# Optimization experiments

Hardware: AMD Instinct MI355X
Metric: run time of the kernel (lower is better)

## Reference

```python
import jax, jax.numpy as jnp
import numpy as np

N = 262144          # num keyframes
E = 1048576         # num visual links (edges)
DT = 0.1            # IMU integration step
L1, L2, L3, L4 = 1.0, 0.5, 2.0, 0.5
EPS = 1e-6

# ---- quaternion helpers (pypose convention: q = [x, y, z, w]) ----

def qmul(q1, q2):
    v1, w1 = q1[..., :3], q1[..., 3:4]
    v2, w2 = q2[..., :3], q2[..., 3:4]
    w = w1 * w2 - jnp.sum(v1 * v2, axis=-1, keepdims=True)
    v = w1 * v2 + w2 * v1 + jnp.cross(v1, v2)
    return jnp.concatenate([v, w], axis=-1)

def qconj(q):
    return jnp.concatenate([-q[..., :3], q[..., 3:4]], axis=-1)

def qrot(q, x):
    # rotate vector x by unit quaternion q: x + 2*cross(v, cross(v,x) + w*x)
    v, w = q[..., :3], q[..., 3:4]
    return x + 2.0 * jnp.cross(v, jnp.cross(v, x) + w * x)

def so3_log(q):
    # log map of unit quaternion -> axis-angle phi (..., 3)
    v, w = q[..., :3], q[..., 3:4]
    n = jnp.linalg.norm(v, axis=-1, keepdims=True)
    n_safe = jnp.where(n < EPS, 1.0, n)
    theta = 2.0 * jnp.arctan2(n, w)
    w_safe = jnp.where(jnp.abs(w) < EPS, 1.0, w)
    factor = jnp.where(n < EPS, 2.0 / w_safe, theta / n_safe)
    return factor * v

def se3_inv(p):
    t, q = p[..., :3], p[..., 3:]
    qi = qconj(q)
    ti = -qrot(qi, t)
    return jnp.concatenate([ti, qi], axis=-1)

def se3_mul(p1, p2):
    t1, q1 = p1[..., :3], p1[..., 3:]
    t2, q2 = p2[..., :3], p2[..., 3:]
    t = t1 + qrot(q1, t2)
    return jnp.concatenate([t, qmul(q1, q2)], axis=-1)

def se3_log(p):
    # returns se(3) tensor [tau, phi] (pypose order) with tau = Jl^{-1}(phi) t
    t, q = p[..., :3], p[..., 3:]
    phi = so3_log(q)
    th = jnp.linalg.norm(phi, axis=-1, keepdims=True)
    th_safe = jnp.where(th < EPS, 1.0, th)
    coef = jnp.where(
        th < EPS,
        1.0 / 12.0 + th * th / 720.0,
        1.0 / (th_safe * th_safe)
        - (1.0 + jnp.cos(th_safe)) / (2.0 * th_safe * jnp.sin(th_safe)),
    )
    pxt = jnp.cross(phi, t)
    tau = t - 0.5 * pxt + coef * jnp.cross(phi, pxt)
    return jnp.concatenate([tau, phi], axis=-1)


def setup_inputs() -> dict:
    key = jax.random.key(0)
    ks = jax.random.split(key, 8)

    def unit_quat(k, n):
        q = jax.random.normal(k, (n, 4), dtype=jnp.float32)
        return q / jnp.linalg.norm(q, axis=-1, keepdims=True)

    pose = jnp.concatenate(
        [jax.random.normal(ks[0], (N, 3), dtype=jnp.float32),
         unit_quat(ks[1], N)], axis=-1)
    vel = jax.random.normal(ks[2], (N, 3), dtype=jnp.float32)
    vmot = jnp.concatenate(
        [0.1 * jax.random.normal(ks[3], (E, 3), dtype=jnp.float32),
         unit_quat(ks[4], E)], axis=-1)
    imu_drot = unit_quat(ks[5], N - 1)
    body_dvel = 0.1 * jax.random.normal(ks[6], (N - 1, 3), dtype=jnp.float32)
    body_dpos = 0.1 * jax.random.normal(ks[7], (N - 1, 3), dtype=jnp.float32)
    vlink = jax.random.randint(jax.random.fold_in(key, 99), (E, 2), 0, N)
    return dict(pose=pose, vel=vel, vmot=vmot, imu_drot=imu_drot,
                body_dvel=body_dvel, body_dpos=body_dpos, vlink=vlink)


def reference(pose, vel, vmot, imu_drot, body_dvel, body_dpos, vlink):
    trans, rot = pose[:, :3], pose[:, 3:]
    r1 = rot[:-1]

    # IMU model: world-frame increments (rotation-dependent, as in original)
    imu_dvel = qrot(r1, body_dvel)                      # world_dvel(pose.rotation())
    imu_dpos = qrot(r1, body_dpos) + vel[:-1] * DT      # world_dpos(rot, vel)

    # pose-graph residual: Log(vmot^{-1} @ pose1^{-1} @ pose2)  [E, 6]
    pose1 = pose[vlink[:, 0]]
    pose2 = pose[vlink[:, 1]]
    err = se3_mul(se3_inv(vmot), se3_mul(se3_inv(pose1), pose2))
    pgerr = se3_log(err)

    # adjacent velocity residual [N-1, 3]
    adjvelerr = imu_dvel - jnp.diff(vel, axis=0)

    # IMU rotation residual: Log(imu_drot @ R1^{-1} @ R2)  [N-1, 3]
    q_rel = qmul(imu_drot, qmul(qconj(rot[:-1]), rot[1:]))
    imuroterr = so3_log(q_rel)

    # translation/velocity residual [N-1, 3]
    transvelerr = imu_dpos - jnp.diff(trans, axis=0)

    return jnp.concatenate([
        L1 * pgerr.reshape(-1),
        L2 * adjvelerr.reshape(-1),
        L3 * imuroterr.reshape(-1),
        L4 * transvelerr.reshape(-1),
    ], axis=0)
```

## Files before the change

### kernel.cpp

```cpp
#include <hip/hip_runtime.h>
#include <math.h>

constexpr int   NN  = 262144;
constexpr int   NE  = 1048576;
constexpr float DTc = 0.1f;
constexpr float W1 = 1.0f, W2 = 0.5f, W3 = 2.0f, W4 = 0.5f;
constexpr float EPSc = 1e-6f;

typedef float    __attribute__((ext_vector_type(2))) f32x2;
typedef float    __attribute__((ext_vector_type(4))) f32x4;
typedef float    __attribute__((ext_vector_type(4), aligned(4))) f32x4u;
typedef float    __attribute__((ext_vector_type(2), aligned(4))) f32x2u;
typedef int      __attribute__((ext_vector_type(2))) i32x2;
typedef _Float16 __attribute__((ext_vector_type(8))) f16x8;

struct V3 { float x, y, z; };
struct Q4 { float x, y, z, w; };

__device__ __forceinline__ V3 v3(float x, float y, float z) { V3 r{x, y, z}; return r; }
__device__ __forceinline__ V3 vadd(V3 a, V3 b) { return v3(a.x + b.x, a.y + b.y, a.z + b.z); }
__device__ __forceinline__ V3 vsub(V3 a, V3 b) { return v3(a.x - b.x, a.y - b.y, a.z - b.z); }
__device__ __forceinline__ V3 vscale(float s, V3 a) { return v3(s * a.x, s * a.y, s * a.z); }
__device__ __forceinline__ V3 vcross(V3 a, V3 b) {
    return v3(a.y * b.z - a.z * b.y, a.z * b.x - a.x * b.z, a.x * b.y - a.y * b.x);
}
__device__ __forceinline__ float vdot(V3 a, V3 b) { return a.x * b.x + a.y * b.y + a.z * b.z; }

__device__ __forceinline__ Q4 qmul(Q4 a, Q4 b) {
    Q4 r;
    r.w = a.w * b.w - (a.x * b.x + a.y * b.y + a.z * b.z);
    r.x = a.w * b.x + b.w * a.x + (a.y * b.z - a.z * b.y);
    r.y = a.w * b.y + b.w * a.y + (a.z * b.x - a.x * b.z);
    r.z = a.w * b.z + b.w * a.z + (a.x * b.y - a.y * b.x);
    return r;
}
__device__ __forceinline__ Q4 qconj(Q4 q) { Q4 r{-q.x, -q.y, -q.z, q.w}; return r; }
__device__ __forceinline__ V3 qrot(Q4 q, V3 x) {
    V3 v = v3(q.x, q.y, q.z);
    V3 c1 = vadd(vcross(v, x), vscale(q.w, x));
    return vadd(x, vscale(2.0f, vcross(v, c1)));
}
__device__ __forceinline__ V3 so3_log(Q4 q) {
    V3 v = v3(q.x, q.y, q.z);
    float n = sqrtf(vdot(v, v));
    float theta = 2.0f * atan2f(n, q.w);
    float factor;
    if (n < EPSc) {
        float w_safe = (fabsf(q.w) < EPSc) ? 1.0f : q.w;
        factor = 2.0f / w_safe;
    } else {
        factor = theta / n;
    }
    return vscale(factor, v);
}

__device__ __forceinline__ void edge_residual(V3 tm, Q4 qm, V3 t1, Q4 q1,
                                              V3 t2, Q4 q2, float* __restrict__ o) {
    Q4 qa = qconj(q1);
    V3 ta = vscale(-1.0f, qrot(qa, t1));
    V3 tb = vadd(ta, qrot(qa, t2));
    Q4 qb = qmul(qa, q2);
    Q4 qc = qconj(qm);
    V3 tc = vscale(-1.0f, qrot(qc, tm));
    V3 te = vadd(tc, qrot(qc, tb));
    Q4 qe = qmul(qc, qb);

    V3 phi = so3_log(qe);
    float th = sqrtf(vdot(phi, phi));
    float coef;
    if (th < EPSc) {
        coef = 1.0f / 12.0f + th * th / 720.0f;
    } else {
        float s, c;
        sincosf(th, &s, &c);
        coef = 1.0f / (th * th) - (1.0f + c) / (2.0f * th * s);
    }
    V3 pxt = vcross(phi, te);
    V3 tau = vadd(vsub(te, vscale(0.5f, pxt)), vscale(coef, vcross(phi, pxt)));

    f32x2* o2 = (f32x2*)o;
    f32x2 a = {W1 * tau.x, W1 * tau.y};
    f32x2 b = {W1 * tau.z, W1 * phi.x};
    f32x2 c = {W1 * phi.y, W1 * phi.z};
    __builtin_nontemporal_store(a, o2);
    __builtin_nontemporal_store(b, o2 + 1);
    __builtin_nontemporal_store(c, o2 + 2);
}

__global__ __launch_bounds__(256) void node_pack_kernel(
    const float* __restrict__ pose, const float* __restrict__ vel,
    const float* __restrict__ imu_drot, const float* __restrict__ body_dvel,
    const float* __restrict__ body_dpos, f16x8* __restrict__ ppH,
    float* __restrict__ out)
{
    int i = blockIdx.x * blockDim.x + threadIdx.x;
    if (i >= NN) return;
    f32x4u pa0 = *(const f32x4u*)(pose + 7 * (size_t)i);
    f32x4u pa1 = *(const f32x4u*)(pose + 7 * (size_t)i + 3);
    f16x8 rec = {(_Float16)pa0.x, (_Float16)pa0.y, (_Float16)pa0.z,
                 (_Float16)pa1.x, (_Float16)pa1.y, (_Float16)pa1.z,
                 (_Float16)pa1.w, (_Float16)0.0f};
    ppH[i] = rec;
    if (i >= NN - 1) return;

    V3 tr1 = v3(pa0.x, pa0.y, pa0.z); Q4 r1 = {pa1.x, pa1.y, pa1.z, pa1.w};
    f32x4u pb0 = *(const f32x4u*)(pose + 7 * (size_t)(i + 1));
    f32x4u pb1 = *(const f32x4u*)(pose + 7 * (size_t)(i + 1) + 3);
    V3 tr2 = v3(pb0.x, pb0.y, pb0.z); Q4 r2 = {pb1.x, pb1.y, pb1.z, pb1.w};

    f32x4u vv = *(const f32x4u*)(vel + 3 * (size_t)i);
    f32x2u vw = *(const f32x2u*)(vel + 3 * (size_t)i + 4);
    V3 v1 = v3(vv.x, vv.y, vv.z);
    V3 v2 = v3(vv.w, vw.x, vw.y);
    V3 bdv = v3(body_dvel[3 * (size_t)i], body_dvel[3 * (size_t)i + 1], body_dvel[3 * (size_t)i + 2]);
    V3 bdp = v3(body_dpos[3 * (size_t)i], body_dpos[3 * (size_t)i + 1], body_dpos[3 * (size_t)i + 2]);
    f32x4 id4 = *(const f32x4*)(imu_drot + 4 * (size_t)i);
    Q4 idr = {id4.x, id4.y, id4.z, id4.w};

    V3 imu_dvel = qrot(r1, bdv);
    V3 adjvel = vsub(imu_dvel, vsub(v2, v1));
    Q4 qrel = qmul(idr, qmul(qconj(r1), r2));
    V3 imurot = so3_log(qrel);
    V3 imu_dpos = vadd(qrot(r1, bdp), vscale(DTc, v1));
    V3 transvel = vsub(imu_dpos, vsub(tr2, tr1));

    size_t base = (size_t)6 * NE;
    size_t nm1 = (size_t)(NN - 1);
    float* oa = out + base + 3 * (size_t)i;
    oa[0] = W2 * adjvel.x; oa[1] = W2 * adjvel.y; oa[2] = W2 * adjvel.z;
    float* ob = out + base + 3 * nm1 + 3 * (size_t)i;
    ob[0] = W3 * imurot.x; ob[1] = W3 * imurot.y; ob[2] = W3 * imurot.z;
    float* oc = out + base + 6 * nm1 + 3 * (size_t)i;
    oc[0] = W4 * transvel.x; oc[1] = W4 * transvel.y; oc[2] = W4 * transvel.z;
}

__global__ __launch_bounds__(256) void edge_kernel(
    const float* __restrict__ vmot, const int* __restrict__ vlink,
    const f16x8* __restrict__ ppH, float* __restrict__ out)
{
    __shared__ float smv[256 * 7];
    int e0 = blockIdx.x * 256;
    const f32x4* src = (const f32x4*)(vmot + (size_t)e0 * 7);
    {
        int idx = threadIdx.x;
        ((f32x4*)smv)[idx] = __builtin_nontemporal_load(src + idx);
        idx += 256;
        if (idx < 448) ((f32x4*)smv)[idx] = __builtin_nontemporal_load(src + idx);
    }
    int e = e0 + threadIdx.x;
    i32x2 l = __builtin_nontemporal_load((const i32x2*)vlink + e);
    f16x8 g1 = ppH[l.x];
    f16x8 g2 = ppH[l.y];
    __syncthreads();
    float m[7];
#pragma unroll
    for (int k = 0; k < 7; ++k) m[k] = smv[7 * threadIdx.x + k];

    V3 t1 = v3((float)g1[0], (float)g1[1], (float)g1[2]);
    Q4 q1 = {(float)g1[3], (float)g1[4], (float)g1[5], (float)g1[6]};
    V3 t2 = v3((float)g2[0], (float)g2[1], (float)g2[2]);
    Q4 q2 = {(float)g2[3], (float)g2[4], (float)g2[5], (float)g2[6]};

    edge_residual(v3(m[0], m[1], m[2]), Q4{m[3], m[4], m[5], m[6]},
                  t1, q1, t2, q2, out + 6 * (size_t)e);
}

__global__ __launch_bounds__(256) void vigraph_fallback(
    const float* __restrict__ pose, const float* __restrict__ vel,
    const float* __restrict__ vmot, const float* __restrict__ imu_drot,
    const float* __restrict__ body_dvel, const float* __restrict__ body_dpos,
    const int* __restrict__ vlink, float* __restrict__ out)
{
    int tid = blockIdx.x * blockDim.x + threadIdx.x;
    if (tid < NE) {
        int e = tid;
        const float* pm = vmot + 7 * (size_t)e;
        int i1 = vlink[2 * (size_t)e];
        int i2 = vlink[2 * (size_t)e + 1];
        const float* p1 = pose + 7 * (size_t)i1;
        const float* p2 = pose + 7 * (size_t)i2;
        edge_residual(v3(pm[0], pm[1], pm[2]), Q4{pm[3], pm[4], pm[5], pm[6]},
                      v3(p1[0], p1[1], p1[2]), Q4{p1[3], p1[4], p1[5], p1[6]},
                      v3(p2[0], p2[1], p2[2]), Q4{p2[3], p2[4], p2[5], p2[6]},
                      out + 6 * (size_t)e);
    } else {
        int i = tid - NE;
        if (i >= NN - 1) return;
        const float* pa = pose + 7 * (size_t)i;
        const float* pb = pose + 7 * (size_t)(i + 1);
        V3 tr1 = v3(pa[0], pa[1], pa[2]); Q4 r1 = {pa[3], pa[4], pa[5], pa[6]};
        V3 tr2 = v3(pb[0], pb[1], pb[2]); Q4 r2 = {pb[3], pb[4], pb[5], pb[6]};
        V3 v1 = v3(vel[3 * (size_t)i], vel[3 * (size_t)i + 1], vel[3 * (size_t)i + 2]);
        V3 v2 = v3(vel[3 * (size_t)(i + 1)], vel[3 * (size_t)(i + 1) + 1], vel[3 * (size_t)(i + 1) + 2]);
        V3 bdv = v3(body_dvel[3 * (size_t)i], body_dvel[3 * (size_t)i + 1], body_dvel[3 * (size_t)i + 2]);
        V3 bdp = v3(body_dpos[3 * (size_t)i], body_dpos[3 * (size_t)i + 1], body_dpos[3 * (size_t)i + 2]);
        Q4 idr = {imu_drot[4 * (size_t)i], imu_drot[4 * (size_t)i + 1],
                  imu_drot[4 * (size_t)i + 2], imu_drot[4 * (size_t)i + 3]};
        V3 imu_dvel = qrot(r1, bdv);
        V3 adjvel = vsub(imu_dvel, vsub(v2, v1));
        Q4 qrel = qmul(idr, qmul(qconj(r1), r2));
        V3 imurot = so3_log(qrel);
        V3 imu_dpos = vadd(qrot(r1, bdp), vscale(DTc, v1));
        V3 transvel = vsub(imu_dpos, vsub(tr2, tr1));
        size_t base = (size_t)6 * NE;
        size_t nm1 = (size_t)(NN - 1);
        float* oa = out + base + 3 * (size_t)i;
        oa[0] = W2 * adjvel.x; oa[1] = W2 * adjvel.y; oa[2] = W2 * adjvel.z;
        float* ob = out + base + 3 * nm1 + 3 * (size_t)i;
        ob[0] = W3 * imurot.x; ob[1] = W3 * imurot.y; ob[2] = W3 * imurot.z;
        float* oc = out + base + 6 * nm1 + 3 * (size_t)i;
        oc[0] = W4 * transvel.x; oc[1] = W4 * transvel.y; oc[2] = W4 * transvel.z;
    }
}

extern "C" void kernel_launch(void* const* d_in, const int* in_sizes, int n_in,
                              void* d_out, int out_size, void* d_ws, size_t ws_size,
                              hipStream_t stream) {
    const float* pose      = (const float*)d_in[0];
    const float* vel       = (const float*)d_in[1];
    const float* vmot      = (const float*)d_in[2];
    const float* imu_drot  = (const float*)d_in[3];
    const float* body_dvel = (const float*)d_in[4];
    const float* body_dpos = (const float*)d_in[5];
    const int*   vlink     = (const int*)d_in[6];
    float* out = (float*)d_out;

    const size_t table_bytes = (size_t)NN * 16;
    if (ws_size >= table_bytes) {
        f16x8* ppH = (f16x8*)d_ws;
        node_pack_kernel<<<NN / 256, 256, 0, stream>>>(pose, vel, imu_drot,
                                                       body_dvel, body_dpos, ppH, out);
        edge_kernel<<<NE / 256, 256, 0, stream>>>(vmot, vlink, ppH, out);
    } else {
        int total = NE + (NN - 1);
        int grid = (total + 255) / 256;
        vigraph_fallback<<<grid, 256, 0, stream>>>(pose, vel, vmot, imu_drot,
                                                   body_dvel, body_dpos, vlink, out);
    }
}
```

Measured before the change: 39.06 us.

## Process two edges per thread with direct vmot loads, drop LDS staging

The edge kernel now handles two edges per thread, taken half the edge count apart. It loads vmot directly with unaligned 16-byte nontemporal loads instead of staging it through shared memory with a barrier, and issues all four gathers before computing. This is meant to raise memory-level parallelism and remove the LDS round trip and __syncthreads, at the cost of uncoalesced overlapping vmot loads and half as many threads. The node kernel also merges the body_dvel and body_dpos scalar loads into 2-wide vector loads.

```diff
diff --git a/kernel.cpp b/kernel.cpp
--- a/kernel.cpp
+++ b/kernel.cpp
@@ -3,6 +3,7 @@
 
 constexpr int   NN  = 262144;
 constexpr int   NE  = 1048576;
+constexpr int   NE2 = NE / 2;
 constexpr float DTc = 0.1f;
 constexpr float W1 = 1.0f, W2 = 0.5f, W3 = 2.0f, W4 = 0.5f;
 constexpr float EPSc = 1e-6f;
@@ -112,8 +113,12 @@
     f32x2u vw = *(const f32x2u*)(vel + 3 * (size_t)i + 4);
     V3 v1 = v3(vv.x, vv.y, vv.z);
     V3 v2 = v3(vv.w, vw.x, vw.y);
-    V3 bdv = v3(body_dvel[3 * (size_t)i], body_dvel[3 * (size_t)i + 1], body_dvel[3 * (size_t)i + 2]);
-    V3 bdp = v3(body_dpos[3 * (size_t)i], body_dpos[3 * (size_t)i + 1], body_dpos[3 * (size_t)i + 2]);
+    f32x2u bv0 = *(const f32x2u*)(body_dvel + 3 * (size_t)i);
+    float  bv2 = body_dvel[3 * (size_t)i + 2];
+    f32x2u bp0 = *(const f32x2u*)(body_dpos + 3 * (size_t)i);
+    float  bp2 = body_dpos[3 * (size_t)i + 2];
+    V3 bdv = v3(bv0.x, bv0.y, bv2);
+    V3 bdp = v3(bp0.x, bp0.y, bp2);
     f32x4 id4 = *(const f32x4*)(imu_drot + 4 * (size_t)i);
     Q4 idr = {id4.x, id4.y, id4.z, id4.w};
 
@@ -138,31 +143,33 @@
     const float* __restrict__ vmot, const int* __restrict__ vlink,
     const f16x8* __restrict__ ppH, float* __restrict__ out)
 {
-    __shared__ float smv[256 * 7];
-    int e0 = blockIdx.x * 256;
-    const f32x4* src = (const f32x4*)(vmot + (size_t)e0 * 7);
-    {
-        int idx = threadIdx.x;
-        ((f32x4*)smv)[idx] = __builtin_nontemporal_load(src + idx);
-        idx += 256;
-        if (idx < 448) ((f32x4*)smv)[idx] = __builtin_nontemporal_load(src + idx);
-    }
-    int e = e0 + threadIdx.x;
-    i32x2 l = __builtin_nontemporal_load((const i32x2*)vlink + e);
-    f16x8 g1 = ppH[l.x];
-    f16x8 g2 = ppH[l.y];
-    __syncthreads();
-    float m[7];
-#pragma unroll
-    for (int k = 0; k < 7; ++k) m[k] = smv[7 * threadIdx.x + k];
-
-    V3 t1 = v3((float)g1[0], (float)g1[1], (float)g1[2]);
-    Q4 q1 = {(float)g1[3], (float)g1[4], (float)g1[5], (float)g1[6]};
-    V3 t2 = v3((float)g2[0], (float)g2[1], (float)g2[2]);
-    Q4 q2 = {(float)g2[3], (float)g2[4], (float)g2[5], (float)g2[6]};
-
-    edge_residual(v3(m[0], m[1], m[2]), Q4{m[3], m[4], m[5], m[6]},
-                  t1, q1, t2, q2, out + 6 * (size_t)e);
+    int tid = blockIdx.x * blockDim.x + threadIdx.x;
+    if (tid >= NE2) return;
+    int e0 = tid, e1 = tid + NE2;
+
+    i32x2 l0 = __builtin_nontemporal_load((const i32x2*)vlink + e0);
+    i32x2 l1 = __builtin_nontemporal_load((const i32x2*)vlink + e1);
+    f32x4u m0a = __builtin_nontemporal_load((const f32x4u*)(vmot + 7 * (size_t)e0));
+    f32x4u m0b = __builtin_nontemporal_load((const f32x4u*)(vmot + 7 * (size_t)e0 + 3));
+    f32x4u m1a = __builtin_nontemporal_load((const f32x4u*)(vmot + 7 * (size_t)e1));
+    f32x4u m1b = __builtin_nontemporal_load((const f32x4u*)(vmot + 7 * (size_t)e1 + 3));
+    f16x8 g10 = ppH[l0.x];
+    f16x8 g20 = ppH[l0.y];
+    f16x8 g11 = ppH[l1.x];
+    f16x8 g21 = ppH[l1.y];
+
+    edge_residual(v3(m0a.x, m0a.y, m0a.z), Q4{m0b.x, m0b.y, m0b.z, m0b.w},
+                  v3((float)g10[0], (float)g10[1], (float)g10[2]),
+                  Q4{(float)g10[3], (float)g10[4], (float)g10[5], (float)g10[6]},
+                  v3((float)g20[0], (float)g20[1], (float)g20[2]),
+                  Q4{(float)g20[3], (float)g20[4], (float)g20[5], (float)g20[6]},
+                  out + 6 * (size_t)e0);
+    edge_residual(v3(m1a.x, m1a.y, m1a.z), Q4{m1b.x, m1b.y, m1b.z, m1b.w},
+                  v3((float)g11[0], (float)g11[1], (float)g11[2]),
+                  Q4{(float)g11[3], (float)g11[4], (float)g11[5], (float)g11[6]},
+                  v3((float)g21[0], (float)g21[1], (float)g21[2]),
+                  Q4{(float)g21[3], (float)g21[4], (float)g21[5], (float)g21[6]},
+                  out + 6 * (size_t)e1);
 }
 
 __global__ __launch_bounds__(256) void vigraph_fallback(
@@ -230,7 +237,7 @@
         f16x8* ppH = (f16x8*)d_ws;
         node_pack_kernel<<<NN / 256, 256, 0, stream>>>(pose, vel, imu_drot,
                                                        body_dvel, body_dpos, ppH, out);
-        edge_kernel<<<NE / 256, 256, 0, stream>>>(vmot, vlink, ppH, out);
+        edge_kernel<<<NE2 / 256, 256, 0, stream>>>(vmot, vlink, ppH, out);
     } else {
         int total = NE + (NN - 1);
         int grid = (total + 255) / 256;
```

After: 40.23 us. 1.03x slower.
